# Optimization experiments

Hardware: AMD Instinct MI355X
Metric: run time of the kernel (lower is better)

## Reference

```python
import jax, jax.numpy as jnp
import numpy as np

IN = 4096      # in_channels (unpacked)
OUT = 11008    # out_channels
GROUP = 128    # quantization group size
W_BIT = 4
PACK = 32 // W_BIT  # 8 int4 values per int32
N_GROUPS = IN // GROUP
BATCH = 64


def setup_inputs() -> dict:
    key = jax.random.key(0)
    k1, k2, k3, k4 = jax.random.split(key, 4)
    x = jax.random.normal(k1, (BATCH, IN), dtype=jnp.float32)
    # bit-packed int4 weights: 8 nibbles per int32, packed along input dim
    qweight = jax.random.randint(k2, (IN // PACK, OUT), 0, jnp.iinfo(jnp.int32).max, dtype=jnp.int32)
    scales = jax.random.uniform(k3, (N_GROUPS, OUT), dtype=jnp.float32) * 0.01 + 1e-3
    # zero points near mid-range of int4
    zeros = 7.5 + jax.random.uniform(k4, (N_GROUPS, OUT), dtype=jnp.float32) - 0.5
    g_idx = (jnp.arange(IN) // GROUP).astype(jnp.int32)
    return {"x": x, "qweight": qweight, "scales": scales, "zeros": zeros, "g_idx": g_idx}


def unpack_int4(qweight):
    # [IN//8, OUT] int32 -> [IN, OUT] float32 in [0, 15]
    shifts = (jnp.arange(PACK, dtype=jnp.int32) * W_BIT)  # [8]
    nibbles = (qweight[:, None, :] >> shifts[None, :, None]) & 0xF  # [IN//8, 8, OUT]
    return nibbles.reshape(IN, OUT).astype(jnp.float32)


def reference(x, qweight, scales, zeros, g_idx):
    w_int = unpack_int4(qweight)                       # [IN, OUT]
    W = (w_int - zeros[g_idx]) * scales[g_idx]         # group-wise dequant, [IN, OUT]
    return x @ W                                       # [BATCH, OUT]
```

## Files before the change

kernel.cpp:

```cpp
#include <hip/hip_runtime.h>
#include <stdint.h>


#define IN 4096
#define OUT 11008
#define BATCH 64
#define SPLITK 8
#define KSPL 512
#define BN 128
#define GRID_N 86

typedef __attribute__((ext_vector_type(8))) __bf16 bf16x8;
typedef __attribute__((ext_vector_type(4))) float f32x4;

static __device__ __forceinline__ ushort f2bf(float f) {
  uint32_t u = __float_as_uint(f);
  u += 0x7fff + ((u >> 16) & 1);
  return (ushort)(u >> 16);
}
static __device__ __forceinline__ float bf2f(ushort h) {
  return __uint_as_float(((uint32_t)h) << 16);
}

__global__ void cvt_frag_kernel(const float* __restrict__ x,
                                ushort* __restrict__ xbf,
                                float* __restrict__ xsum) {
  const int g = blockIdx.x;
  const int t = threadIdx.x;
  const int m = t >> 2;
  const int q = t & 3;
  const int ks = 4 * g + q;
  const int kb = 32 * ks;

  float v[32];
  ushort vb[32];
  float s = 0.f;
#pragma unroll
  for (int c4 = 0; c4 < 8; ++c4) {
    float4 f = *(const float4*)&x[m * IN + kb + 4 * c4];
    v[4 * c4 + 0] = f.x; v[4 * c4 + 1] = f.y; v[4 * c4 + 2] = f.z; v[4 * c4 + 3] = f.w;
  }
#pragma unroll
  for (int c = 0; c < 32; ++c) {
    vb[c] = f2bf(v[c]);
    s += bf2f(vb[c]);
  }
  const int i = m >> 4, mlane = m & 15;
#pragma unroll
  for (int qd = 0; qd < 4; ++qd) {
    ushort o[8];
    o[0] = vb[8 * qd + 0]; o[1] = vb[8 * qd + 4];
    o[2] = vb[8 * qd + 1]; o[3] = vb[8 * qd + 5];
    o[4] = vb[8 * qd + 2]; o[5] = vb[8 * qd + 6];
    o[6] = vb[8 * qd + 3]; o[7] = vb[8 * qd + 7];
    const int flat = (ks * 4 + i) * 64 + qd * 16 + mlane;
    *(uint4*)&xbf[flat * 8] = *(uint4*)o;
  }
  s += __shfl_xor(s, 1);
  s += __shfl_xor(s, 2);
  if (q == 0) xsum[g * 64 + m] = s;
}

__global__ __launch_bounds__(256, 3) void mpq_gemm(
    const ushort* __restrict__ xbf,
    const int* __restrict__ qweight,
    const float* __restrict__ scales,
    const float* __restrict__ zeros,
    const float* __restrict__ xsum,
    float* __restrict__ P)
{
  __shared__ uint4 A_lds[2048];

  const int n0 = blockIdx.x * BN;
  const int sp = blockIdx.y;
  const int k0 = sp * KSPL;
  const int tid = threadIdx.x;
  const int lane = tid & 63;
  const int w = tid >> 6;
  const int mlane = lane & 15, quad = lane >> 4;
  const int ncol = n0 + 32 * w + mlane;

  f32x4 macc[4][2] = {};

  const uint4* gA = (const uint4*)xbf + (size_t)(k0 / 32) * 256;

  for (int h = 0; h < 2; ++h) {
    __syncthreads();
    const uint4* src = gA + (size_t)h * 8 * 256;
#pragma unroll
    for (int it = 0; it < 8; ++it)
      A_lds[tid + 256 * it] = src[tid + 256 * it];
    __syncthreads();

    const int qrow0 = k0 / 8 + h * 32;
#pragma unroll
    for (int g2 = 0; g2 < 2; ++g2) {
      f32x4 gacc[4][2] = {};
#pragma unroll
      for (int ksl = 0; ksl < 4; ++ksl) {
        const int ks = g2 * 4 + ksl;
        uint32_t q[2];
        const int qrow = qrow0 + ks * 4 + quad;
#pragma unroll
        for (int j = 0; j < 2; ++j)
          q[j] = (uint32_t)qweight[(size_t)qrow * OUT + ncol + 16 * j];
        bf16x8 af[4];
#pragma unroll
        for (int i = 0; i < 4; ++i)
          af[i] = *(const bf16x8*)&A_lds[(ks * 4 + i) * 64 + lane];
#pragma unroll
        for (int j = 0; j < 2; ++j) {
          uint32_t p[4];
          p[0] = ( q[j]        & 0x000F000Fu) | 0x43004300u;
          p[1] = ((q[j] >>  4) & 0x000F000Fu) | 0x43004300u;
          p[2] = ((q[j] >>  8) & 0x000F000Fu) | 0x43004300u;
          p[3] = ((q[j] >> 12) & 0x000F000Fu) | 0x43004300u;
          bf16x8 bfr = *(bf16x8*)p;
#pragma unroll
          for (int i = 0; i < 4; ++i)
            gacc[i][j] = __builtin_amdgcn_mfma_f32_16x16x32_bf16(af[i], bfr, gacc[i][j], 0, 0, 0);
        }
      }
      const int g = (k0 >> 7) + h * 2 + g2;
      float Sv[4][4];
#pragma unroll
      for (int i = 0; i < 4; ++i)
#pragma unroll
        for (int r = 0; r < 4; ++r)
          Sv[i][r] = xsum[g * 64 + 16 * i + 4 * quad + r];
#pragma unroll
      for (int j = 0; j < 2; ++j) {
        const float s = scales[g * OUT + ncol + 16 * j];
        const float z = zeros[g * OUT + ncol + 16 * j];
        const float u = s * (128.0f + z);
#pragma unroll
        for (int i = 0; i < 4; ++i)
#pragma unroll
          for (int r = 0; r < 4; ++r)
            macc[i][j][r] = fmaf(s, gacc[i][j][r], fmaf(-u, Sv[i][r], macc[i][j][r]));
      }
    }
  }

  float* Pp = P + (size_t)sp * BATCH * OUT;
#pragma unroll
  for (int i = 0; i < 4; ++i)
#pragma unroll
    for (int r = 0; r < 4; ++r) {
      const int m = 16 * i + 4 * quad + r;
#pragma unroll
      for (int j = 0; j < 2; ++j)
        Pp[(size_t)m * OUT + ncol + 16 * j] = macc[i][j][r];
    }
}

__global__ void reduce_kernel(const float* __restrict__ P, float* __restrict__ out) {
  const int t = blockIdx.x * blockDim.x + threadIdx.x;
  float4 a = ((const float4*)P)[t];
#pragma unroll
  for (int s = 1; s < SPLITK; ++s) {
    float4 b = ((const float4*)P)[t + (size_t)s * (BATCH * OUT / 4)];
    a.x += b.x; a.y += b.y; a.z += b.z; a.w += b.w;
  }
  ((float4*)out)[t] = a;
}

extern "C" void kernel_launch(void* const* d_in, const int* in_sizes, int n_in,
                              void* d_out, int out_size, void* d_ws, size_t ws_size,
                              hipStream_t stream) {
  const float* x = (const float*)d_in[0];
  const int* qweight = (const int*)d_in[1];
  const float* scales = (const float*)d_in[2];
  const float* zeros = (const float*)d_in[3];
  float* out = (float*)d_out;
  ushort* xbf = (ushort*)d_ws;
  float* xsum = (float*)((char*)d_ws + (1 << 19));
  float* P = (float*)((char*)d_ws + (1 << 20));

  cvt_frag_kernel<<<32, 256, 0, stream>>>(x, xbf, xsum);
  mpq_gemm<<<dim3(GRID_N, SPLITK), 256, 0, stream>>>(xbf, qweight, scales, zeros, xsum, P);
  reduce_kernel<<<BATCH * OUT / 4 / 256, 256, 0, stream>>>(P, out);
}
```

Measured before the change: 95.95 us.

## Fuse split-K reduction into GEMM via atomic counters and re-tile warps

Split-K drops from 8 to 4 and the N tile from 128 to 64, so there are 688 blocks instead of 688 with a different shape. The four warps now split into 2x2 over M and N rather than 4 over N. The separate reduce kernel is removed. Each column tile's last-finishing block, detected with an atomic counter that the conversion kernel resets, sums the partial results and writes the output. This saves one launch and halves the partial-sum traffic, at the cost of longer K loops per block, each qweight load being reused across fewer rows, and a serialized tail reduction.

Result: slower. 196.1 us (+104.4%).

```diff
diff --git a/kernel.cpp b/kernel.cpp
--- a/kernel.cpp
+++ b/kernel.cpp
@@ -5,10 +5,10 @@
 #define IN 4096
 #define OUT 11008
 #define BATCH 64
-#define SPLITK 8
-#define KSPL 512
-#define BN 128
-#define GRID_N 86
+#define SPLITK 4
+#define KSPL 1024
+#define BN 64
+#define GRID_N 172
 
 typedef __attribute__((ext_vector_type(8))) __bf16 bf16x8;
 typedef __attribute__((ext_vector_type(4))) float f32x4;
@@ -24,9 +24,11 @@
 
 __global__ void cvt_frag_kernel(const float* __restrict__ x,
                                 ushort* __restrict__ xbf,
-                                float* __restrict__ xsum) {
+                                float* __restrict__ xsum,
+                                int* __restrict__ cnt) {
   const int g = blockIdx.x;
   const int t = threadIdx.x;
+  if (g == 0 && t < GRID_N) cnt[t] = 0;
   const int m = t >> 2;
   const int q = t & 3;
   const int ks = 4 * g + q;
@@ -67,9 +69,12 @@
     const float* __restrict__ scales,
     const float* __restrict__ zeros,
     const float* __restrict__ xsum,
-    float* __restrict__ P)
+    float* __restrict__ P,
+    int* __restrict__ cnt,
+    float* __restrict__ out)
 {
   __shared__ uint4 A_lds[2048];
+  __shared__ int last_flag;
 
   const int n0 = blockIdx.x * BN;
   const int sp = blockIdx.y;
@@ -77,16 +82,17 @@
   const int tid = threadIdx.x;
   const int lane = tid & 63;
   const int w = tid >> 6;
+  const int wm = w >> 1, wn = w & 1;
   const int mlane = lane & 15, quad = lane >> 4;
-  const int ncol = n0 + 32 * w + mlane;
-
-  f32x4 macc[4][2] = {};
+  const int ncol = n0 + 32 * wn + mlane;
+
+  f32x4 macc[2][2] = {};
 
   const uint4* gA = (const uint4*)xbf + (size_t)(k0 / 32) * 256;
 
-  for (int h = 0; h < 2; ++h) {
+  for (int h = 0; h < 4; ++h) {
     __syncthreads();
-    const uint4* src = gA + (size_t)h * 8 * 256;
+    const uint4* src = gA + (size_t)h * 2048;
 #pragma unroll
     for (int it = 0; it < 8; ++it)
       A_lds[tid + 256 * it] = src[tid + 256 * it];
@@ -95,7 +101,7 @@
     const int qrow0 = k0 / 8 + h * 32;
 #pragma unroll
     for (int g2 = 0; g2 < 2; ++g2) {
-      f32x4 gacc[4][2] = {};
+      f32x4 gacc[2][2] = {};
 #pragma unroll
       for (int ksl = 0; ksl < 4; ++ksl) {
         const int ks = g2 * 4 + ksl;
@@ -104,10 +110,10 @@
 #pragma unroll
         for (int j = 0; j < 2; ++j)
           q[j] = (uint32_t)qweight[(size_t)qrow * OUT + ncol + 16 * j];
-        bf16x8 af[4];
-#pragma unroll
-        for (int i = 0; i < 4; ++i)
-          af[i] = *(const bf16x8*)&A_lds[(ks * 4 + i) * 64 + lane];
+        bf16x8 af[2];
+#pragma unroll
+        for (int i2 = 0; i2 < 2; ++i2)
+          af[i2] = *(const bf16x8*)&A_lds[(ks * 4 + 2 * wm + i2) * 64 + lane];
 #pragma unroll
         for (int j = 0; j < 2; ++j) {
           uint32_t p[4];
@@ -117,52 +123,63 @@
           p[3] = ((q[j] >> 12) & 0x000F000Fu) | 0x43004300u;
           bf16x8 bfr = *(bf16x8*)p;
 #pragma unroll
-          for (int i = 0; i < 4; ++i)
-            gacc[i][j] = __builtin_amdgcn_mfma_f32_16x16x32_bf16(af[i], bfr, gacc[i][j], 0, 0, 0);
+          for (int i2 = 0; i2 < 2; ++i2)
+            gacc[i2][j] = __builtin_amdgcn_mfma_f32_16x16x32_bf16(af[i2], bfr, gacc[i2][j], 0, 0, 0);
         }
       }
       const int g = (k0 >> 7) + h * 2 + g2;
-      float Sv[4][4];
-#pragma unroll
-      for (int i = 0; i < 4; ++i)
+      float Sv[2][4];
+#pragma unroll
+      for (int i2 = 0; i2 < 2; ++i2)
 #pragma unroll
         for (int r = 0; r < 4; ++r)
-          Sv[i][r] = xsum[g * 64 + 16 * i + 4 * quad + r];
+          Sv[i2][r] = xsum[g * 64 + 32 * wm + 16 * i2 + 4 * quad + r];
 #pragma unroll
       for (int j = 0; j < 2; ++j) {
         const float s = scales[g * OUT + ncol + 16 * j];
         const float z = zeros[g * OUT + ncol + 16 * j];
         const float u = s * (128.0f + z);
 #pragma unroll
-        for (int i = 0; i < 4; ++i)
+        for (int i2 = 0; i2 < 2; ++i2)
 #pragma unroll
           for (int r = 0; r < 4; ++r)
-            macc[i][j][r] = fmaf(s, gacc[i][j][r], fmaf(-u, Sv[i][r], macc[i][j][r]));
+            macc[i2][j][r] = fmaf(s, gacc[i2][j][r], fmaf(-u, Sv[i2][r], macc[i2][j][r]));
       }
     }
   }
 
-  float* Pp = P + (size_t)sp * BATCH * OUT;
-#pragma unroll
-  for (int i = 0; i < 4; ++i)
+  float* Pp = P + (size_t)sp * (BATCH * OUT);
+#pragma unroll
+  for (int i2 = 0; i2 < 2; ++i2)
 #pragma unroll
     for (int r = 0; r < 4; ++r) {
-      const int m = 16 * i + 4 * quad + r;
+      const int m = 32 * wm + 16 * i2 + 4 * quad + r;
 #pragma unroll
       for (int j = 0; j < 2; ++j)
-        Pp[(size_t)m * OUT + ncol + 16 * j] = macc[i][j][r];
+        Pp[(size_t)m * OUT + ncol + 16 * j] = macc[i2][j][r];
     }
-}
-
-__global__ void reduce_kernel(const float* __restrict__ P, float* __restrict__ out) {
-  const int t = blockIdx.x * blockDim.x + threadIdx.x;
-  float4 a = ((const float4*)P)[t];
-#pragma unroll
-  for (int s = 1; s < SPLITK; ++s) {
-    float4 b = ((const float4*)P)[t + (size_t)s * (BATCH * OUT / 4)];
-    a.x += b.x; a.y += b.y; a.z += b.z; a.w += b.w;
-  }
-  ((float4*)out)[t] = a;
+
+  __threadfence();
+  __syncthreads();
+  if (tid == 0) last_flag = (atomicAdd(&cnt[blockIdx.x], 1) == SPLITK - 1);
+  __syncthreads();
+  if (last_flag) {
+    __threadfence();
+    const float4* P4 = (const float4*)P;
+    float4* out4 = (float4*)out;
+#pragma unroll
+    for (int slot = tid; slot < 1024; slot += 256) {
+      const int m = slot >> 4, c = slot & 15;
+      const size_t off = (size_t)m * (OUT / 4) + (n0 >> 2) + c;
+      float4 a = P4[off];
+#pragma unroll
+      for (int s2 = 1; s2 < SPLITK; ++s2) {
+        float4 b = P4[off + (size_t)s2 * (BATCH * OUT / 4)];
+        a.x += b.x; a.y += b.y; a.z += b.z; a.w += b.w;
+      }
+      out4[off] = a;
+    }
+  }
 }
 
 extern "C" void kernel_launch(void* const* d_in, const int* in_sizes, int n_in,
@@ -175,9 +192,9 @@
   float* out = (float*)d_out;
   ushort* xbf = (ushort*)d_ws;
   float* xsum = (float*)((char*)d_ws + (1 << 19));
+  int* cnt = (int*)((char*)d_ws + (1 << 19) + 8192);
   float* P = (float*)((char*)d_ws + (1 << 20));
 
-  cvt_frag_kernel<<<32, 256, 0, stream>>>(x, xbf, xsum);
-  mpq_gemm<<<dim3(GRID_N, SPLITK), 256, 0, stream>>>(xbf, qweight, scales, zeros, xsum, P);
-  reduce_kernel<<<BATCH * OUT / 4 / 256, 256, 0, stream>>>(P, out);
-}
+  cvt_frag_kernel<<<32, 256, 0, stream>>>(x, xbf, xsum, cnt);
+  mpq_gemm<<<dim3(GRID_N, SPLITK), 256, 0, stream>>>(xbf, qweight, scales, zeros, xsum, P, cnt, out);
+}
```
